# Performance work log

Hardware: AMD Instinct MI355X
Metric: run time of the kernel (lower is better)

Reference implementation:

```python
import jax, jax.numpy as jnp
import numpy as np

EMBED_DIM = 1024
NUM_HEADS = 16
HEAD_DIM = EMBED_DIM // NUM_HEADS
B, S = 4, 2048


def setup_inputs() -> dict:
    key = jax.random.key(0)
    ks = jax.random.split(key, 9)
    scale = 1.0 / np.sqrt(EMBED_DIM)
    x = jax.random.normal(ks[0], (B, S, EMBED_DIM), dtype=jnp.float32)
    Wq = jax.random.uniform(ks[1], (EMBED_DIM, EMBED_DIM), jnp.float32, -scale, scale)
    bq = jax.random.uniform(ks[2], (EMBED_DIM,), jnp.float32, -scale, scale)
    Wk = jax.random.uniform(ks[3], (EMBED_DIM, EMBED_DIM), jnp.float32, -scale, scale)
    bk = jax.random.uniform(ks[4], (EMBED_DIM,), jnp.float32, -scale, scale)
    Wv = jax.random.uniform(ks[5], (EMBED_DIM, EMBED_DIM), jnp.float32, -scale, scale)
    bv = jax.random.uniform(ks[6], (EMBED_DIM,), jnp.float32, -scale, scale)
    Wo = jax.random.uniform(ks[7], (EMBED_DIM, EMBED_DIM), jnp.float32, -scale, scale)
    bo = jax.random.uniform(ks[8], (EMBED_DIM,), jnp.float32, -scale, scale)
    return {"x": x, "Wq": Wq, "bq": bq, "Wk": Wk, "bk": bk, "Wv": Wv, "bv": bv, "Wo": Wo, "bo": bo}


def reference(x, Wq, bq, Wk, bk, Wv, bv, Wo, bo):
    b, s, d = x.shape
    h, hd = NUM_HEADS, HEAD_DIM
    # projections -> [b, h, s, hd]
    def proj(W, bias):
        return (x @ W + bias).reshape(b, s, h, hd).transpose(0, 2, 1, 3)
    q = proj(Wq, bq)
    k = proj(Wk, bk)
    v = proj(Wv, bv)
    logits = jnp.einsum('bhqd,bhkd->bhqk', q, k) / np.sqrt(hd).astype(np.float32)
    attn = jax.nn.softmax(logits, axis=-1)  # dropout p=0.0 -> identity
    vals = jnp.einsum('bhqk,bhkd->bhqd', attn, v)
    vals = vals.transpose(0, 2, 1, 3).reshape(b, s, d)
    return vals @ Wo + bo
```

## Files before the change

kernel.cpp:

```cpp
#include <hip/hip_runtime.h>

typedef unsigned short u16;
typedef unsigned int u32;
typedef __bf16 bf16x8 __attribute__((ext_vector_type(8)));
typedef float f32x4 __attribute__((ext_vector_type(4)));
typedef float f32x16 __attribute__((ext_vector_type(16)));
typedef u32 u32x4 __attribute__((ext_vector_type(4)));
typedef u32 u32x2 __attribute__((ext_vector_type(2)));

#define NBATCH 4
#define NS 2048
#define ND 1024
#define NH 16
#define HDIM 64
#define KSCALE (0.125f * 1.44269504f)

#define MFMA(a, b, c) __builtin_amdgcn_mfma_f32_16x16x32_bf16(a, b, c, 0, 0, 0)
#define MFMA32(a, b, c) __builtin_amdgcn_mfma_f32_32x32x16_bf16(a, b, c, 0, 0, 0)

__device__ __forceinline__ u16 f2bf(float f) {
    u32 u = __builtin_bit_cast(u32, f);
    u += 0x7fffu + ((u >> 16) & 1u);
    return (u16)(u >> 16);
}

__device__ __forceinline__ u32 cvtpk(float a, float b) {
    u32 r;
    asm("v_cvt_pk_bf16_f32 %0, %1, %2" : "=v"(r) : "v"(a), "v"(b));
    return r;
}

__device__ __forceinline__ bf16x8 ldfrag(const u16* p) {
    u32x4 v = *(const u32x4*)p;
    return __builtin_bit_cast(bf16x8, v);
}

__device__ __forceinline__ void gld16(u16* lds, const u16* g) {
    __builtin_amdgcn_global_load_lds((__attribute__((address_space(1))) u32*)g,
                                     (__attribute__((address_space(3))) u32*)lds, 16, 0, 0);
}


__global__ __launch_bounds__(256) void cvt_tile(const float* __restrict__ src, u16* __restrict__ dst) {
    const int tile = blockIdx.x;
    const int mt = tile >> 5, ktile = tile & 31;
    const int tid = threadIdx.x;
    u16* out = dst + (size_t)tile * 4096;
#pragma unroll
    for (int half = 0; half < 2; ++half) {
        const int s = half * 256 + tid;
        const int rg = s >> 6, l = s & 63;
        const int row = mt * 128 + rg * 16 + (l & 15);
        const int col = ktile * 32 + (l >> 4) * 8;
        const float* sp = src + (size_t)row * ND + col;
        float4 v0 = *(const float4*)sp;
        float4 v1 = *(const float4*)(sp + 4);
        u32x4 o;
        o[0] = (u32)f2bf(v0.x) | ((u32)f2bf(v0.y) << 16);
        o[1] = (u32)f2bf(v0.z) | ((u32)f2bf(v0.w) << 16);
        o[2] = (u32)f2bf(v1.x) | ((u32)f2bf(v1.y) << 16);
        o[3] = (u32)f2bf(v1.z) | ((u32)f2bf(v1.w) << 16);
        *(u32x4*)(out + s * 8) = o;
    }
}

__global__ __launch_bounds__(256) void wtrans4(const float* __restrict__ W0, const float* __restrict__ W1,
                                               const float* __restrict__ W2, const float* __restrict__ W3,
                                               u16* __restrict__ T0, u16* __restrict__ T1,
                                               u16* __restrict__ T2, u16* __restrict__ T3) {
    const int z = blockIdx.z;
    const float* W = z == 0 ? W0 : z == 1 ? W1 : z == 2 ? W2 : W3;
    u16* WT = z == 0 ? T0 : z == 1 ? T1 : z == 2 ? T2 : T3;
    __shared__ u16 t[64][72];
    const int tid = threadIdx.x;
    const int k0 = blockIdx.x * 64, n0 = blockIdx.y * 64;
    {
        const int r = tid >> 2, cq = (tid & 3) * 16;
#pragma unroll
        for (int i = 0; i < 4; ++i) {
            float4 v = *(const float4*)(W + (size_t)(k0 + r) * ND + n0 + cq + i * 4);
            t[r][cq + i * 4 + 0] = f2bf(v.x);
            t[r][cq + i * 4 + 1] = f2bf(v.y);
            t[r][cq + i * 4 + 2] = f2bf(v.z);
            t[r][cq + i * 4 + 3] = f2bf(v.w);
        }
    }
    __syncthreads();
    {
        const int rr = tid >> 2, cq = (tid & 3) * 16;
        u32x4 o0, o1;
#pragma unroll
        for (int j = 0; j < 4; ++j) {
            o0[j] = (u32)t[cq + 2 * j][rr] | ((u32)t[cq + 2 * j + 1][rr] << 16);
            o1[j] = (u32)t[cq + 8 + 2 * j][rr] | ((u32)t[cq + 8 + 2 * j + 1][rr] << 16);
        }
        const int n_g = n0 + rr;
        const int nt = n_g >> 7, rgn = (n_g >> 4) & 7, lr = n_g & 15;
        const int k_g = k0 + cq;
        const int kt2 = k_g >> 5, lg = (k_g >> 3) & 3;
        u16* outb = WT + ((size_t)(nt * 32 + kt2)) * 4096 + rgn * 512 + lr * 8;
        *(u32x4*)(outb + lg * 128) = o0;
        *(u32x4*)(outb + (lg + 1) * 128) = o1;
    }
}

__global__ __launch_bounds__(256) void gemm_qkv(const u16* __restrict__ A,
                                                const u16* __restrict__ wqT, const u16* __restrict__ wkT,
                                                const u16* __restrict__ wvT,
                                                const float* __restrict__ bq, const float* __restrict__ bk,
                                                const float* __restrict__ bv,
                                                u16* __restrict__ Qp, u16* __restrict__ Kf,
                                                u16* __restrict__ Vf) {
    __shared__ u16 la[8192];
    __shared__ u16 lb[8192];
    const int wg = blockIdx.x;
    const int xcd = wg & 7, idx = wg >> 3;
    const int ybl = xcd * 8 + idx / 24;
    const int xbl = idx % 24;
    const int region = xbl >> 3;
    const int m0 = ybl * 128, n0 = (xbl & 7) * 128;
    const u16* Bt = region == 0 ? wqT : region == 1 ? wkT : wvT;
    const float* bias = region == 0 ? bq : region == 1 ? bk : bv;

    const int tid = threadIdx.x;
    const int l = tid & 63, w = tid >> 6;
    const int lr = l & 15, lg = l >> 4;
    const int wr = w >> 1, wc = w & 1;

    const u16* Atiles = A + (size_t)ybl * 32 * 4096;
    const u16* Btiles = Bt + (size_t)(xbl & 7) * 32 * 4096;

    gld16(la + tid * 8, Atiles + tid * 8);
    gld16(la + (256 + tid) * 8, Atiles + (256 + tid) * 8);
    gld16(lb + tid * 8, Btiles + tid * 8);
    gld16(lb + (256 + tid) * 8, Btiles + (256 + tid) * 8);
    __syncthreads();

    f32x4 acc[4][4] = {};

    for (int kt = 0; kt < 32; ++kt) {
        const int cur = kt & 1;
        if (kt < 31) {
            const u16* ag = Atiles + (size_t)(kt + 1) * 4096;
            const u16* bg = Btiles + (size_t)(kt + 1) * 4096;
            u16* ad = la + (cur ^ 1) * 4096;
            u16* bd = lb + (cur ^ 1) * 4096;
            gld16(ad + tid * 8, ag + tid * 8);
            gld16(ad + (256 + tid) * 8, ag + (256 + tid) * 8);
            gld16(bd + tid * 8, bg + tid * 8);
            gld16(bd + (256 + tid) * 8, bg + (256 + tid) * 8);
        }
        const u16* al = la + cur * 4096;
        const u16* bl = lb + cur * 4096;

        bf16x8 af[4], bv4[4];
#pragma unroll
        for (int mb = 0; mb < 4; ++mb) af[mb] = ldfrag(al + ((wr * 4 + mb) * 64 + l) * 8);
#pragma unroll
        for (int nb = 0; nb < 4; ++nb) bv4[nb] = ldfrag(bl + ((wc * 4 + nb) * 64 + l) * 8);

        __builtin_amdgcn_s_setprio(1);
#pragma unroll
        for (int mb = 0; mb < 4; ++mb)
#pragma unroll
            for (int nb = 0; nb < 4; ++nb)
                acc[mb][nb] = MFMA(af[mb], bv4[nb], acc[mb][nb]);
        __builtin_amdgcn_s_setprio(0);

        __syncthreads();
    }

#pragma unroll
    for (int mb = 0; mb < 4; ++mb) {
#pragma unroll
        for (int nb = 0; nb < 4; ++nb) {
            const int col = n0 + wc * 64 + nb * 16 + lr;
            const float bia = bias[col];
            const int hd = col & 63, h = col >> 6;
            if (region == 2) {
                const int rowb = m0 + wr * 64 + mb * 16 + lg * 4;
                const int b = rowb >> 11, kv = rowb & 2047;
                const int bh = b * NH + h;
                const int ktp = kv >> 6, ks = (kv >> 4) & 3, hif = (kv >> 3) & 1, j0 = kv & 7;
                const int lane = (hd & 31) | (hif << 5);
                u32x2 o;
                o[0] = (u32)f2bf(acc[mb][nb][0] + bia) | ((u32)f2bf(acc[mb][nb][1] + bia) << 16);
                o[1] = (u32)f2bf(acc[mb][nb][2] + bia) | ((u32)f2bf(acc[mb][nb][3] + bia) << 16);
                size_t off = (size_t)bh * 131072 + (size_t)ktp * 4096 +
                             (size_t)(((ks + 4 * (hd >> 5)) * 64 + lane) * 8 + j0);
                *(u32x2*)(Vf + off) = o;
            } else if (region == 1) {
#pragma unroll
                for (int r = 0; r < 4; ++r) {
                    const int rowg = m0 + wr * 64 + mb * 16 + lg * 4 + r;
                    float v = (acc[mb][nb][r] + bia) * KSCALE;
                    const int b = rowg >> 11, kv = rowg & 2047;
                    const int bh = b * NH + h;
                    const int ktp = kv >> 6, kvb = (kv >> 5) & 1;
                    const int lane = (kv & 31) | (((hd >> 3) & 1) << 5);
                    size_t o = (size_t)bh * 131072 + (size_t)ktp * 4096 +
                               (size_t)(((kvb * 4 + (hd >> 4)) * 64 + lane) * 8 + (hd & 7));
                    Kf[o] = f2bf(v);
                }
            } else {
#pragma unroll
                for (int r = 0; r < 4; ++r) {
                    const int rowg = m0 + wr * 64 + mb * 16 + lg * 4 + r;
                    float v = acc[mb][nb][r] + bia;
                    size_t o = ((size_t)((rowg >> 11) * NH + h) * NS + (rowg & 2047)) * HDIM + hd;
                    Qp[o] = f2bf(v);
                }
            }
        }
    }
}

__global__ __launch_bounds__(256) void gemm_o(const u16* __restrict__ A, const u16* __restrict__ Bt,
                                              const float* __restrict__ bias, float* __restrict__ of32) {
    __shared__ u16 la[8192];
    __shared__ u16 lb[8192];
    const int wg = blockIdx.x;
    const int xcd = wg & 7, idx = wg >> 3;
    const int ybl = xcd * 8 + (idx >> 3);
    const int xbl = idx & 7;
    const int m0 = ybl * 128, n0 = xbl * 128;

    const int tid = threadIdx.x;
    const int l = tid & 63, w = tid >> 6;
    const int lr = l & 15, lg = l >> 4;
    const int wr = w >> 1, wc = w & 1;

    const u16* Atiles = A + (size_t)ybl * 32 * 4096;
    const u16* Btiles = Bt + (size_t)xbl * 32 * 4096;

    gld16(la + tid * 8, Atiles + tid * 8);
    gld16(la + (256 + tid) * 8, Atiles + (256 + tid) * 8);
    gld16(lb + tid * 8, Btiles + tid * 8);
    gld16(lb + (256 + tid) * 8, Btiles + (256 + tid) * 8);
    __syncthreads();

    f32x4 acc[4][4] = {};

    for (int kt = 0; kt < 32; ++kt) {
        const int cur = kt & 1;
        if (kt < 31) {
            const u16* ag = Atiles + (size_t)(kt + 1) * 4096;
            const u16* bg = Btiles + (size_t)(kt + 1) * 4096;
            u16* ad = la + (cur ^ 1) * 4096;
            u16* bd = lb + (cur ^ 1) * 4096;
            gld16(ad + tid * 8, ag + tid * 8);
            gld16(ad + (256 + tid) * 8, ag + (256 + tid) * 8);
            gld16(bd + tid * 8, bg + tid * 8);
            gld16(bd + (256 + tid) * 8, bg + (256 + tid) * 8);
        }
        const u16* al = la + cur * 4096;
        const u16* bl = lb + cur * 4096;

        bf16x8 af[4], bv4[4];
#pragma unroll
        for (int mb = 0; mb < 4; ++mb) af[mb] = ldfrag(al + ((wr * 4 + mb) * 64 + l) * 8);
#pragma unroll
        for (int nb = 0; nb < 4; ++nb) bv4[nb] = ldfrag(bl + ((wc * 4 + nb) * 64 + l) * 8);

        __builtin_amdgcn_s_setprio(1);
#pragma unroll
        for (int mb = 0; mb < 4; ++mb)
#pragma unroll
            for (int nb = 0; nb < 4; ++nb)
                acc[mb][nb] = MFMA(af[mb], bv4[nb], acc[mb][nb]);
        __builtin_amdgcn_s_setprio(0);

        __syncthreads();
    }

#pragma unroll
    for (int mb = 0; mb < 4; ++mb) {
#pragma unroll
        for (int nb = 0; nb < 4; ++nb) {
            const int col = n0 + wc * 64 + nb * 16 + lr;
            const float bia = bias[col];
#pragma unroll
            for (int r = 0; r < 4; ++r) {
                const int rowg = m0 + wr * 64 + mb * 16 + lg * 4 + r;
                of32[(size_t)rowg * ND + col] = acc[mb][nb][r] + bia;
            }
        }
    }
}

__global__ __launch_bounds__(256, 3) void attn(const u16* __restrict__ Q, const u16* __restrict__ Kf,
                                               const u16* __restrict__ Vf, u16* __restrict__ AO) {
    __shared__ u16 sm[16384];
    const int tid = threadIdx.x;
    const int l = tid & 63, w = tid >> 6;
    const int lq = l & 31, hi = l >> 5;
    const int wg = blockIdx.x;
    const int xcd = wg & 7, idx = wg >> 3;
    const int bh = xcd * 8 + (idx >> 4);
    const int qb = idx & 15;
    const int qbase = qb * 128 + w * 32;

    const u16* Qrow = Q + ((size_t)bh * NS + qbase + lq) * HDIM;
    bf16x8 qf[4];
#pragma unroll
    for (int kh = 0; kh < 4; ++kh) qf[kh] = ldfrag(Qrow + kh * 16 + hi * 8);

    f32x16 oacc[2] = {};
    float ls0 = 0.f, ls1 = 0.f, ls2 = 0.f, ls3 = 0.f;

    const u16* KfB = Kf + (size_t)bh * 131072;
    const u16* VfB = Vf + (size_t)bh * 131072;

    gld16(sm + tid * 8, KfB + tid * 8);
    gld16(sm + (256 + tid) * 8, KfB + (256 + tid) * 8);
    gld16(sm + 8192 + tid * 8, VfB + tid * 8);
    gld16(sm + 8192 + (256 + tid) * 8, VfB + (256 + tid) * 8);
    __syncthreads();

    for (int kt = 0; kt < 32; ++kt) {
        const int cur = kt & 1;
        if (kt < 31) {
            const u16* kg = KfB + (size_t)(kt + 1) * 4096;
            const u16* vg = VfB + (size_t)(kt + 1) * 4096;
            u16* kd = sm + (cur ^ 1) * 4096;
            u16* vd = sm + 8192 + (cur ^ 1) * 4096;
            gld16(kd + tid * 8, kg + tid * 8);
            gld16(kd + (256 + tid) * 8, kg + (256 + tid) * 8);
            gld16(vd + tid * 8, vg + tid * 8);
            gld16(vd + (256 + tid) * 8, vg + (256 + tid) * 8);
        }
        const u16* klb = sm + cur * 4096;
        const u16* vlb = sm + 8192 + cur * 4096;

        bf16x8 kf[2][4];
#pragma unroll
        for (int kvb = 0; kvb < 2; ++kvb)
#pragma unroll
            for (int kh = 0; kh < 4; ++kh)
                kf[kvb][kh] = ldfrag(klb + ((kvb * 4 + kh) * 64 + l) * 8);

        f32x16 sacc[2] = {};
        __builtin_amdgcn_s_setprio(1);
#pragma unroll
        for (int kvb = 0; kvb < 2; ++kvb)
#pragma unroll
            for (int kh = 0; kh < 4; ++kh)
                sacc[kvb] = MFMA32(kf[kvb][kh], qf[kh], sacc[kvb]);
        __builtin_amdgcn_s_setprio(0);

        bf16x8 vf[2][4];
#pragma unroll
        for (int hdb = 0; hdb < 2; ++hdb)
#pragma unroll
            for (int ks = 0; ks < 4; ++ks)
                vf[hdb][ks] = ldfrag(vlb + ((hdb * 4 + ks) * 64 + l) * 8);

#pragma unroll
        for (int kvb = 0; kvb < 2; ++kvb) {
#pragma unroll
            for (int i = 0; i < 16; i += 4) {
                float p0 = __builtin_amdgcn_exp2f(sacc[kvb][i + 0]);
                float p1 = __builtin_amdgcn_exp2f(sacc[kvb][i + 1]);
                float p2 = __builtin_amdgcn_exp2f(sacc[kvb][i + 2]);
                float p3 = __builtin_amdgcn_exp2f(sacc[kvb][i + 3]);
                sacc[kvb][i + 0] = p0;
                sacc[kvb][i + 1] = p1;
                sacc[kvb][i + 2] = p2;
                sacc[kvb][i + 3] = p3;
                ls0 += p0;
                ls1 += p1;
                ls2 += p2;
                ls3 += p3;
            }
        }

        bf16x8 pf[4];
#pragma unroll
        for (int ks = 0; ks < 4; ++ks) {
            const int i0 = 2 * ks, i1 = 2 * ks + 1;
            const int q20 = i0 & 3, kvb0 = i0 >> 2;
            const int q21 = i1 & 3, kvb1 = i1 >> 2;
            u32 W00 = cvtpk(sacc[kvb0][4 * q20 + 0], sacc[kvb0][4 * q20 + 1]);
            u32 W01 = cvtpk(sacc[kvb0][4 * q20 + 2], sacc[kvb0][4 * q20 + 3]);
            u32 W10 = cvtpk(sacc[kvb1][4 * q21 + 0], sacc[kvb1][4 * q21 + 1]);
            u32 W11 = cvtpk(sacc[kvb1][4 * q21 + 2], sacc[kvb1][4 * q21 + 3]);
            u32x2 s0 = __builtin_amdgcn_permlane32_swap(W00, W10, false, false);
            u32x2 s1 = __builtin_amdgcn_permlane32_swap(W01, W11, false, false);
            u32x4 words;
            words[0] = s0[0];
            words[1] = s1[0];
            words[2] = s0[1];
            words[3] = s1[1];
            pf[ks] = __builtin_bit_cast(bf16x8, words);
        }

        __builtin_amdgcn_s_setprio(1);
#pragma unroll
        for (int hdb = 0; hdb < 2; ++hdb)
#pragma unroll
            for (int ks = 0; ks < 4; ++ks)
                oacc[hdb] = MFMA32(vf[hdb][ks], pf[ks], oacc[hdb]);
        __builtin_amdgcn_s_setprio(0);

        __syncthreads();
    }

    float lsum = (ls0 + ls1) + (ls2 + ls3);
    lsum += __shfl_xor(lsum, 32);

    u16* ot = sm + w * 2048;
    const float inv = 1.f / lsum;
#pragma unroll
    for (int hdb = 0; hdb < 2; ++hdb)
#pragma unroll
        for (int q2 = 0; q2 < 4; ++q2)
#pragma unroll
            for (int rp = 0; rp < 2; ++rp) {
                u32 word = cvtpk(oacc[hdb][4 * q2 + 2 * rp] * inv, oacc[hdb][4 * q2 + 2 * rp + 1] * inv);
                const int hd0 = hdb * 32 + 8 * q2 + 4 * hi + 2 * rp;
                const int byteoff = lq * 128 + ((2 * hd0) ^ ((lq & 7) << 4));
                *(u32*)((char*)ot + byteoff) = word;
            }
    const int b = bh >> 4, h = bh & 15;
#pragma unroll
    for (int p = 0; p < 4; ++p) {
        const int pidx = p * 64 + l;
        const int row = pidx >> 3;
        const int cb = ((pidx & 7) * 16) ^ ((row & 7) << 4);
        u32x4 val = *(u32x4*)((char*)ot + row * 128 + cb);
        const int m = b * NS + qbase + row;
        const int c = h * 64 + (pidx & 7) * 8;
        const int mt = m >> 7, rg = (m >> 4) & 7, lrm = m & 15;
        const int ktile = c >> 5, lgc = (c >> 3) & 3;
        *(u32x4*)(AO + ((size_t)(mt * 32 + ktile)) * 4096 + rg * 512 + (lgc * 16 + lrm) * 8) = val;
    }
}

extern "C" void kernel_launch(void* const* d_in, const int* in_sizes, int n_in,
                              void* d_out, int out_size, void* d_ws, size_t ws_size,
                              hipStream_t stream) {
    const float* x = (const float*)d_in[0];
    const float* Wq = (const float*)d_in[1];
    const float* bq = (const float*)d_in[2];
    const float* Wk = (const float*)d_in[3];
    const float* bk = (const float*)d_in[4];
    const float* Wv = (const float*)d_in[5];
    const float* bv = (const float*)d_in[6];
    const float* Wo = (const float*)d_in[7];
    const float* bo = (const float*)d_in[8];
    float* out = (float*)d_out;

    u16* ws = (u16*)d_ws;
    u16* xb = ws;
    u16* wqT = ws + 8388608;
    u16* wkT = wqT + 1048576;
    u16* wvT = wkT + 1048576;
    u16* woT = wvT + 1048576;
    u16* Qp = woT + 1048576;
    u16* Kfp = Qp + 8388608;
    u16* Vfp = Kfp + 8388608;
    u16* AO = xb;

    cvt_tile<<<2048, 256, 0, stream>>>(x, xb);
    wtrans4<<<dim3(16, 16, 4), 256, 0, stream>>>(Wq, Wk, Wv, Wo, wqT, wkT, wvT, woT);
    gemm_qkv<<<1536, 256, 0, stream>>>(xb, wqT, wkT, wvT, bq, bk, bv, Qp, Kfp, Vfp);
    attn<<<1024, 256, 0, stream>>>(Qp, Kfp, Vfp, AO);
    gemm_o<<<512, 256, 0, stream>>>(AO, woT, bo, out);
}
```

Baseline: 201.5 us.

## Load MFMA fragments directly from global into registers, drop LDS staging

Replaces the LDS double-buffered global_load_lds staging in the QKV GEMM, output GEMM and attention kernels with direct per-wave global loads of MFMA fragments into registers. Register double buffering prefetches the next K-tile while the current one is multiplied. This removes the per-iteration __syncthreads and LDS traffic, and lets the GEMMs request three blocks per CU. In exchange, each wave that shares an operand tile re-reads it from global/L2 instead of sharing one LDS copy, which raises cache traffic and exposes more global latency.

```diff
diff --git a/kernel.cpp b/kernel.cpp
--- a/kernel.cpp
+++ b/kernel.cpp
@@ -33,11 +33,6 @@
 __device__ __forceinline__ bf16x8 ldfrag(const u16* p) {
     u32x4 v = *(const u32x4*)p;
     return __builtin_bit_cast(bf16x8, v);
-}
-
-__device__ __forceinline__ void gld16(u16* lds, const u16* g) {
-    __builtin_amdgcn_global_load_lds((__attribute__((address_space(1))) u32*)g,
-                                     (__attribute__((address_space(3))) u32*)lds, 16, 0, 0);
 }
 
 
@@ -104,15 +99,36 @@
     }
 }
 
-__global__ __launch_bounds__(256) void gemm_qkv(const u16* __restrict__ A,
-                                                const u16* __restrict__ wqT, const u16* __restrict__ wkT,
-                                                const u16* __restrict__ wvT,
-                                                const float* __restrict__ bq, const float* __restrict__ bk,
-                                                const float* __restrict__ bv,
-                                                u16* __restrict__ Qp, u16* __restrict__ Kf,
-                                                u16* __restrict__ Vf) {
-    __shared__ u16 la[8192];
-    __shared__ u16 lb[8192];
+template <bool PF>
+__device__ __forceinline__ void gemm_step(const bf16x8 (&a)[4], const bf16x8 (&b)[4],
+                                          bf16x8 (&an)[4], bf16x8 (&bn)[4],
+                                          const u16* aw, const u16* bw, int kt,
+                                          f32x4 (&acc)[4][4]) {
+    if (PF) {
+        const u16* ap = aw + (size_t)(kt + 1) * 4096;
+        const u16* bp = bw + (size_t)(kt + 1) * 4096;
+#pragma unroll
+        for (int i = 0; i < 4; ++i) {
+            an[i] = ldfrag(ap + i * 512);
+            bn[i] = ldfrag(bp + i * 512);
+        }
+    }
+    __builtin_amdgcn_s_setprio(1);
+#pragma unroll
+    for (int mb = 0; mb < 4; ++mb)
+#pragma unroll
+        for (int nb = 0; nb < 4; ++nb)
+            acc[mb][nb] = MFMA(a[mb], b[nb], acc[mb][nb]);
+    __builtin_amdgcn_s_setprio(0);
+}
+
+__global__ __launch_bounds__(256, 3) void gemm_qkv(const u16* __restrict__ A,
+                                                   const u16* __restrict__ wqT, const u16* __restrict__ wkT,
+                                                   const u16* __restrict__ wvT,
+                                                   const float* __restrict__ bq, const float* __restrict__ bk,
+                                                   const float* __restrict__ bv,
+                                                   u16* __restrict__ Qp, u16* __restrict__ Kf,
+                                                   u16* __restrict__ Vf) {
     const int wg = blockIdx.x;
     const int xcd = wg & 7, idx = wg >> 3;
     const int ybl = xcd * 8 + idx / 24;
@@ -127,47 +143,23 @@
     const int lr = l & 15, lg = l >> 4;
     const int wr = w >> 1, wc = w & 1;
 
-    const u16* Atiles = A + (size_t)ybl * 32 * 4096;
-    const u16* Btiles = Bt + (size_t)(xbl & 7) * 32 * 4096;
-
-    gld16(la + tid * 8, Atiles + tid * 8);
-    gld16(la + (256 + tid) * 8, Atiles + (256 + tid) * 8);
-    gld16(lb + tid * 8, Btiles + tid * 8);
-    gld16(lb + (256 + tid) * 8, Btiles + (256 + tid) * 8);
-    __syncthreads();
+    const u16* aw = A + (size_t)ybl * 32 * 4096 + wr * 2048 + l * 8;
+    const u16* bw = Bt + (size_t)(xbl & 7) * 32 * 4096 + wc * 2048 + l * 8;
 
     f32x4 acc[4][4] = {};
-
-    for (int kt = 0; kt < 32; ++kt) {
-        const int cur = kt & 1;
-        if (kt < 31) {
-            const u16* ag = Atiles + (size_t)(kt + 1) * 4096;
-            const u16* bg = Btiles + (size_t)(kt + 1) * 4096;
-            u16* ad = la + (cur ^ 1) * 4096;
-            u16* bd = lb + (cur ^ 1) * 4096;
-            gld16(ad + tid * 8, ag + tid * 8);
-            gld16(ad + (256 + tid) * 8, ag + (256 + tid) * 8);
-            gld16(bd + tid * 8, bg + tid * 8);
-            gld16(bd + (256 + tid) * 8, bg + (256 + tid) * 8);
-        }
-        const u16* al = la + cur * 4096;
-        const u16* bl = lb + cur * 4096;
-
-        bf16x8 af[4], bv4[4];
-#pragma unroll
-        for (int mb = 0; mb < 4; ++mb) af[mb] = ldfrag(al + ((wr * 4 + mb) * 64 + l) * 8);
-#pragma unroll
-        for (int nb = 0; nb < 4; ++nb) bv4[nb] = ldfrag(bl + ((wc * 4 + nb) * 64 + l) * 8);
-
-        __builtin_amdgcn_s_setprio(1);
-#pragma unroll
-        for (int mb = 0; mb < 4; ++mb)
-#pragma unroll
-            for (int nb = 0; nb < 4; ++nb)
-                acc[mb][nb] = MFMA(af[mb], bv4[nb], acc[mb][nb]);
-        __builtin_amdgcn_s_setprio(0);
-
-        __syncthreads();
+    bf16x8 aA[4], bA[4], aB[4], bB[4];
+#pragma unroll
+    for (int i = 0; i < 4; ++i) {
+        aA[i] = ldfrag(aw + i * 512);
+        bA[i] = ldfrag(bw + i * 512);
+    }
+
+    for (int kt = 0; kt < 32; kt += 2) {
+        gemm_step<true>(aA, bA, aB, bB, aw, bw, kt, acc);
+        if (kt + 2 < 32)
+            gemm_step<true>(aB, bB, aA, bA, aw, bw, kt + 1, acc);
+        else
+            gemm_step<false>(aB, bB, aA, bA, aw, bw, kt + 1, acc);
     }
 
 #pragma unroll
@@ -215,10 +207,8 @@
     }
 }
 
-__global__ __launch_bounds__(256) void gemm_o(const u16* __restrict__ A, const u16* __restrict__ Bt,
-                                              const float* __restrict__ bias, float* __restrict__ of32) {
-    __shared__ u16 la[8192];
-    __shared__ u16 lb[8192];
+__global__ __launch_bounds__(256, 3) void gemm_o(const u16* __restrict__ A, const u16* __restrict__ Bt,
+                                                 const float* __restrict__ bias, float* __restrict__ of32) {
     const int wg = blockIdx.x;
     const int xcd = wg & 7, idx = wg >> 3;
     const int ybl = xcd * 8 + (idx >> 3);
@@ -230,47 +220,23 @@
     const int lr = l & 15, lg = l >> 4;
     const int wr = w >> 1, wc = w & 1;
 
-    const u16* Atiles = A + (size_t)ybl * 32 * 4096;
-    const u16* Btiles = Bt + (size_t)xbl * 32 * 4096;
-
-    gld16(la + tid * 8, Atiles + tid * 8);
-    gld16(la + (256 + tid) * 8, Atiles + (256 + tid) * 8);
-    gld16(lb + tid * 8, Btiles + tid * 8);
-    gld16(lb + (256 + tid) * 8, Btiles + (256 + tid) * 8);
-    __syncthreads();
+    const u16* aw = A + (size_t)ybl * 32 * 4096 + wr * 2048 + l * 8;
+    const u16* bw = Bt + (size_t)xbl * 32 * 4096 + wc * 2048 + l * 8;
 
     f32x4 acc[4][4] = {};
-
-    for (int kt = 0; kt < 32; ++kt) {
-        const int cur = kt & 1;
-        if (kt < 31) {
-            const u16* ag = Atiles + (size_t)(kt + 1) * 4096;
-            const u16* bg = Btiles + (size_t)(kt + 1) * 4096;
-            u16* ad = la + (cur ^ 1) * 4096;
-            u16* bd = lb + (cur ^ 1) * 4096;
-            gld16(ad + tid * 8, ag + tid * 8);
-            gld16(ad + (256 + tid) * 8, ag + (256 + tid) * 8);
-            gld16(bd + tid * 8, bg + tid * 8);
-            gld16(bd + (256 + tid) * 8, bg + (256 + tid) * 8);
-        }
-        const u16* al = la + cur * 4096;
-        const u16* bl = lb + cur * 4096;
-
-        bf16x8 af[4], bv4[4];
-#pragma unroll
-        for (int mb = 0; mb < 4; ++mb) af[mb] = ldfrag(al + ((wr * 4 + mb) * 64 + l) * 8);
-#pragma unroll
-        for (int nb = 0; nb < 4; ++nb) bv4[nb] = ldfrag(bl + ((wc * 4 + nb) * 64 + l) * 8);
-
-        __builtin_amdgcn_s_setprio(1);
-#pragma unroll
-        for (int mb = 0; mb < 4; ++mb)
-#pragma unroll
-            for (int nb = 0; nb < 4; ++nb)
-                acc[mb][nb] = MFMA(af[mb], bv4[nb], acc[mb][nb]);
-        __builtin_amdgcn_s_setprio(0);
-
-        __syncthreads();
+    bf16x8 aA[4], bA[4], aB[4], bB[4];
+#pragma unroll
+    for (int i = 0; i < 4; ++i) {
+        aA[i] = ldfrag(aw + i * 512);
+        bA[i] = ldfrag(bw + i * 512);
+    }
+
+    for (int kt = 0; kt < 32; kt += 2) {
+        gemm_step<true>(aA, bA, aB, bB, aw, bw, kt, acc);
+        if (kt + 2 < 32)
+            gemm_step<true>(aB, bB, aA, bA, aw, bw, kt + 1, acc);
+        else
+            gemm_step<false>(aB, bB, aA, bA, aw, bw, kt + 1, acc);
     }
 
 #pragma unroll
@@ -288,9 +254,82 @@
     }
 }
 
+template <bool PF>
+__device__ __forceinline__ void attn_step(const bf16x8 (&kf)[8], bf16x8 (&kfn)[8],
+                                          const u16* kw, const u16* vw, int kt,
+                                          const bf16x8 (&qf)[4], f32x16 (&oacc)[2],
+                                          float& ls0, float& ls1, float& ls2, float& ls3) {
+    if (PF) {
+        const u16* kp = kw + (size_t)(kt + 1) * 4096;
+#pragma unroll
+        for (int i = 0; i < 8; ++i) kfn[i] = ldfrag(kp + i * 512);
+    }
+
+    f32x16 sacc[2] = {};
+    __builtin_amdgcn_s_setprio(1);
+#pragma unroll
+    for (int kvb = 0; kvb < 2; ++kvb)
+#pragma unroll
+        for (int kh = 0; kh < 4; ++kh)
+            sacc[kvb] = MFMA32(kf[kvb * 4 + kh], qf[kh], sacc[kvb]);
+    __builtin_amdgcn_s_setprio(0);
+
+    bf16x8 vf[8];
+    const u16* vp = vw + (size_t)kt * 4096;
+#pragma unroll
+    for (int i = 0; i < 8; ++i) vf[i] = ldfrag(vp + i * 512);
+
+#pragma unroll
+    for (int kvb = 0; kvb < 2; ++kvb) {
+#pragma unroll
+        for (int i = 0; i < 16; i += 4) {
+            float p0 = __builtin_amdgcn_exp2f(sacc[kvb][i + 0]);
+            float p1 = __builtin_amdgcn_exp2f(sacc[kvb][i + 1]);
+            float p2 = __builtin_amdgcn_exp2f(sacc[kvb][i + 2]);
+            float p3 = __builtin_amdgcn_exp2f(sacc[kvb][i + 3]);
+            sacc[kvb][i + 0] = p0;
+            sacc[kvb][i + 1] = p1;
+            sacc[kvb][i + 2] = p2;
+            sacc[kvb][i + 3] = p3;
+            ls0 += p0;
+            ls1 += p1;
+            ls2 += p2;
+            ls3 += p3;
+        }
+    }
+
+    bf16x8 pf[4];
+#pragma unroll
+    for (int ks = 0; ks < 4; ++ks) {
+        const int i0 = 2 * ks, i1 = 2 * ks + 1;
+        const int q20 = i0 & 3, kvb0 = i0 >> 2;
+        const int q21 = i1 & 3, kvb1 = i1 >> 2;
+        u32 W00 = cvtpk(sacc[kvb0][4 * q20 + 0], sacc[kvb0][4 * q20 + 1]);
+        u32 W01 = cvtpk(sacc[kvb0][4 * q20 + 2], sacc[kvb0][4 * q20 + 3]);
+        u32 W10 = cvtpk(sacc[kvb1][4 * q21 + 0], sacc[kvb1][4 * q21 + 1]);
+        u32 W11 = cvtpk(sacc[kvb1][4 * q21 + 2], sacc[kvb1][4 * q21 + 3]);
+        u32x2 s0 = __builtin_amdgcn_permlane32_swap(W00, W10, false, false);
+        u32x2 s1 = __builtin_amdgcn_permlane32_swap(W01, W11, false, false);
+        u32x4 words;
+        words[0] = s0[0];
+        words[1] = s1[0];
+        words[2] = s0[1];
+        words[3] = s1[1];
+        pf[ks] = __builtin_bit_cast(bf16x8, words);
+    }
+
+    __builtin_amdgcn_s_setprio(1);
+#pragma unroll
+    for (int hdb = 0; hdb < 2; ++hdb)
+#pragma unroll
+        for (int ks = 0; ks < 4; ++ks)
+            oacc[hdb] = MFMA32(vf[hdb * 4 + ks], pf[ks], oacc[hdb]);
+    __builtin_amdgcn_s_setprio(0);
+}
+
 __global__ __launch_bounds__(256, 3) void attn(const u16* __restrict__ Q, const u16* __restrict__ Kf,
                                                const u16* __restrict__ Vf, u16* __restrict__ AO) {
-    __shared__ u16 sm[16384];
+    __shared__ u16 sm[8192];
     const int tid = threadIdx.x;
     const int l = tid & 63, w = tid >> 6;
     const int lq = l & 31, hi = l >> 5;
@@ -308,101 +347,19 @@
     f32x16 oacc[2] = {};
     float ls0 = 0.f, ls1 = 0.f, ls2 = 0.f, ls3 = 0.f;
 
-    const u16* KfB = Kf + (size_t)bh * 131072;
-    const u16* VfB = Vf + (size_t)bh * 131072;
-
-    gld16(sm + tid * 8, KfB + tid * 8);
-    gld16(sm + (256 + tid) * 8, KfB + (256 + tid) * 8);
-    gld16(sm + 8192 + tid * 8, VfB + tid * 8);
-    gld16(sm + 8192 + (256 + tid) * 8, VfB + (256 + tid) * 8);
-    __syncthreads();
-
-    for (int kt = 0; kt < 32; ++kt) {
-        const int cur = kt & 1;
-        if (kt < 31) {
-            const u16* kg = KfB + (size_t)(kt + 1) * 4096;
-            const u16* vg = VfB + (size_t)(kt + 1) * 4096;
-            u16* kd = sm + (cur ^ 1) * 4096;
-            u16* vd = sm + 8192 + (cur ^ 1) * 4096;
-            gld16(kd + tid * 8, kg + tid * 8);
-            gld16(kd + (256 + tid) * 8, kg + (256 + tid) * 8);
-            gld16(vd + tid * 8, vg + tid * 8);
-            gld16(vd + (256 + tid) * 8, vg + (256 + tid) * 8);
-        }
-        const u16* klb = sm + cur * 4096;
-        const u16* vlb = sm + 8192 + cur * 4096;
-
-        bf16x8 kf[2][4];
-#pragma unroll
-        for (int kvb = 0; kvb < 2; ++kvb)
-#pragma unroll
-            for (int kh = 0; kh < 4; ++kh)
-                kf[kvb][kh] = ldfrag(klb + ((kvb * 4 + kh) * 64 + l) * 8);
-
-        f32x16 sacc[2] = {};
-        __builtin_amdgcn_s_setprio(1);
-#pragma unroll
-        for (int kvb = 0; kvb < 2; ++kvb)
-#pragma unroll
-            for (int kh = 0; kh < 4; ++kh)
-                sacc[kvb] = MFMA32(kf[kvb][kh], qf[kh], sacc[kvb]);
-        __builtin_amdgcn_s_setprio(0);
-
-        bf16x8 vf[2][4];
-#pragma unroll
-        for (int hdb = 0; hdb < 2; ++hdb)
-#pragma unroll
-            for (int ks = 0; ks < 4; ++ks)
-                vf[hdb][ks] = ldfrag(vlb + ((hdb * 4 + ks) * 64 + l) * 8);
-
-#pragma unroll
-        for (int kvb = 0; kvb < 2; ++kvb) {
-#pragma unroll
-            for (int i = 0; i < 16; i += 4) {
-                float p0 = __builtin_amdgcn_exp2f(sacc[kvb][i + 0]);
-                float p1 = __builtin_amdgcn_exp2f(sacc[kvb][i + 1]);
-                float p2 = __builtin_amdgcn_exp2f(sacc[kvb][i + 2]);
-                float p3 = __builtin_amdgcn_exp2f(sacc[kvb][i + 3]);
-                sacc[kvb][i + 0] = p0;
-                sacc[kvb][i + 1] = p1;
-                sacc[kvb][i + 2] = p2;
-                sacc[kvb][i + 3] = p3;
-                ls0 += p0;
-                ls1 += p1;
-                ls2 += p2;
-                ls3 += p3;
-            }
-        }
-
-        bf16x8 pf[4];
-#pragma unroll
-        for (int ks = 0; ks < 4; ++ks) {
-            const int i0 = 2 * ks, i1 = 2 * ks + 1;
-            const int q20 = i0 & 3, kvb0 = i0 >> 2;
-            const int q21 = i1 & 3, kvb1 = i1 >> 2;
-            u32 W00 = cvtpk(sacc[kvb0][4 * q20 + 0], sacc[kvb0][4 * q20 + 1]);
-            u32 W01 = cvtpk(sacc[kvb0][4 * q20 + 2], sacc[kvb0][4 * q20 + 3]);
-            u32 W10 = cvtpk(sacc[kvb1][4 * q21 + 0], sacc[kvb1][4 * q21 + 1]);
-            u32 W11 = cvtpk(sacc[kvb1][4 * q21 + 2], sacc[kvb1][4 * q21 + 3]);
-            u32x2 s0 = __builtin_amdgcn_permlane32_swap(W00, W10, false, false);
-            u32x2 s1 = __builtin_amdgcn_permlane32_swap(W01, W11, false, false);
-            u32x4 words;
-            words[0] = s0[0];
-            words[1] = s1[0];
-            words[2] = s0[1];
-            words[3] = s1[1];
-            pf[ks] = __builtin_bit_cast(bf16x8, words);
-        }
-
-        __builtin_amdgcn_s_setprio(1);
-#pragma unroll
-        for (int hdb = 0; hdb < 2; ++hdb)
-#pragma unroll
-            for (int ks = 0; ks < 4; ++ks)
-                oacc[hdb] = MFMA32(vf[hdb][ks], pf[ks], oacc[hdb]);
-        __builtin_amdgcn_s_setprio(0);
-
-        __syncthreads();
+    const u16* kw = Kf + (size_t)bh * 131072 + l * 8;
+    const u16* vw = Vf + (size_t)bh * 131072 + l * 8;
+
+    bf16x8 kfA[8], kfB[8];
+#pragma unroll
+    for (int i = 0; i < 8; ++i) kfA[i] = ldfrag(kw + i * 512);
+
+    for (int kt = 0; kt < 32; kt += 2) {
+        attn_step<true>(kfA, kfB, kw, vw, kt, qf, oacc, ls0, ls1, ls2, ls3);
+        if (kt + 2 < 32)
+            attn_step<true>(kfB, kfA, kw, vw, kt + 1, qf, oacc, ls0, ls1, ls2, ls3);
+        else
+            attn_step<false>(kfB, kfA, kw, vw, kt + 1, qf, oacc, ls0, ls1, ls2, ls3);
     }
 
     float lsum = (ls0 + ls1) + (ls2 + ls3);
```

Result: slower. 330.7 us (+64.1%).
